# Performance work log

Hardware: AMD Instinct MI355X
Metric: run time of the kernel (lower is better)

## Reference

```python
import jax, jax.numpy as jnp
import numpy as np
from jax import lax

N_NODES = 100000
N_EDGES = 600000  # even: edges stored as consecutive reverse pairs
NODE_F = 64
EDGE_F = 16
EDGE_H = 128
NODE_H = 128
NUM_STEPS = 6


def setup_inputs() -> dict:
    key = jax.random.key(0)
    ks = jax.random.split(key, 16)
    # paired reverse edges: edge 2k is (src,dst), edge 2k+1 is (dst,src)
    src = jax.random.randint(ks[0], (N_EDGES // 2,), 0, N_NODES, dtype=jnp.int32)
    dst = jax.random.randint(ks[1], (N_EDGES // 2,), 0, N_NODES, dtype=jnp.int32)
    from_nodes = jnp.stack([src, dst], axis=1).reshape(-1)
    to_nodes = jnp.stack([dst, src], axis=1).reshape(-1)
    edges = jnp.stack([from_nodes, to_nodes], axis=0)
    return {
        "node_features": jax.random.normal(ks[2], (N_NODES, NODE_F), jnp.float32),
        "edge_features": jax.random.normal(ks[3], (N_EDGES, EDGE_F), jnp.float32),
        "edge_hiddens": jnp.zeros((N_EDGES, EDGE_H), jnp.float32),
        "edges": edges,
        "W1_w": jax.random.normal(ks[4], (NODE_F, EDGE_H), jnp.float32) / np.sqrt(NODE_F),
        "W1_b": jnp.zeros((EDGE_H,), jnp.float32),
        "W2_w": jax.random.normal(ks[5], (EDGE_F, EDGE_H), jnp.float32) / np.sqrt(EDGE_F),
        "W2_b": jnp.zeros((EDGE_H,), jnp.float32),
        "W3_w": jax.random.normal(ks[6], (EDGE_H, EDGE_H), jnp.float32) / np.sqrt(EDGE_H),
        "W3_b": jnp.zeros((EDGE_H,), jnp.float32),
        "U1_w": jax.random.normal(ks[7], (NODE_F, NODE_H), jnp.float32) / np.sqrt(NODE_F),
        "U1_b": jnp.zeros((NODE_H,), jnp.float32),
        "U2_w": jax.random.normal(ks[8], (EDGE_H, NODE_H), jnp.float32) / np.sqrt(EDGE_H),
        "U2_b": jnp.zeros((NODE_H,), jnp.float32),
    }


def reference(node_features, edge_features, edge_hiddens, edges,
              W1_w, W1_b, W2_w, W2_b, W3_w, W3_b, U1_w, U1_b, U2_w, U2_b):
    from_nodes = edges[0]
    to_nodes = edges[1]
    n_edges = edges.shape[1]
    # backlink of edge i is its reverse pair: even i -> i+1, odd i -> i-1
    idx = jnp.arange(n_edges)
    backlink = idx + ((idx + 1) % 2) * 2 - 1

    # loop-invariant terms
    W1_x_u = (node_features @ W1_w + W1_b)[from_nodes]     # [E, EH]
    W2_x_uv = edge_features @ W2_w + W2_b                  # [E, EH]

    def step(h, _):
        # sum edge hiddens by source node, gather back per-edge, drop backlink
        s = jax.ops.segment_sum(h, from_nodes, num_segments=N_NODES)  # [N, EH]
        wu = s[from_nodes] - h[backlink]                               # [E, EH]
        h_new = jax.nn.relu(W1_x_u + W2_x_uv + (wu @ W3_w + W3_b))
        return h_new, None

    edge_h, _ = lax.scan(step, edge_hiddens, None, length=NUM_STEPS)

    U1_x_u = node_features @ U1_w + U1_b                   # [N, NH]
    U2_vu = edge_h @ U2_w + U2_b                           # [E, NH]
    agg = jax.ops.segment_sum(U2_vu, to_nodes, num_segments=N_NODES)
    node_hiddens = jax.nn.relu(U1_x_u + agg)               # [N, NH]
    return node_hiddens
```

## Files before the change

kernel.cpp:

```cpp
#include <hip/hip_runtime.h>
#include <hip/hip_bf16.h>

#define N_NODES 100000
#define N_EDGES 600000
#define SCAN_BLOCKS ((N_NODES + 255) / 256)

typedef __bf16 bf16;
typedef __bf16 bf16x2 __attribute__((ext_vector_type(2)));
typedef __bf16 bf16x4 __attribute__((ext_vector_type(4)));
typedef __bf16 bf16x8 __attribute__((ext_vector_type(8)));
typedef float f32x4 __attribute__((ext_vector_type(4)));

__global__ void deg_hist(const int* __restrict__ from, int* __restrict__ deg, int E) {
    int e = blockIdx.x * blockDim.x + threadIdx.x;
    if (e < E) atomicAdd(&deg[from[e]], 1);
}

__global__ __launch_bounds__(256) void block_sums(
    const int* __restrict__ deg, int* __restrict__ bsum)
{
    __shared__ int s[256];
    int i = blockIdx.x * 256 + threadIdx.x;
    s[threadIdx.x] = (i < N_NODES) ? deg[i] : 0;
    __syncthreads();
    for (int st = 128; st > 0; st >>= 1) {
        if (threadIdx.x < st) s[threadIdx.x] += s[threadIdx.x + st];
        __syncthreads();
    }
    if (threadIdx.x == 0) bsum[blockIdx.x] = s[0];
}

__global__ __launch_bounds__(256) void scan_partials(
    const int* __restrict__ bsum, int* __restrict__ bpref, int* __restrict__ off)
{
    __shared__ int s[SCAN_BLOCKS];
    for (int i = threadIdx.x; i < SCAN_BLOCKS; i += 256) s[i] = bsum[i];
    __syncthreads();
    if (threadIdx.x == 0) {
        int run = 0;
        for (int i = 0; i < SCAN_BLOCKS; i++) { int t = s[i]; s[i] = run; run += t; }
        off[N_NODES] = run;
    }
    __syncthreads();
    for (int i = threadIdx.x; i < SCAN_BLOCKS; i += 256) bpref[i] = s[i];
}

__global__ __launch_bounds__(256) void block_scan(
    const int* __restrict__ deg, const int* __restrict__ bpref,
    int* __restrict__ off, int* __restrict__ cursor)
{
    __shared__ int s[256];
    int i = blockIdx.x * 256 + threadIdx.x;
    int v = (i < N_NODES) ? deg[i] : 0;
    s[threadIdx.x] = v;
    __syncthreads();
    for (int st = 1; st < 256; st <<= 1) {
        int x = (threadIdx.x >= st) ? s[threadIdx.x - st] : 0;
        __syncthreads();
        s[threadIdx.x] += x;
        __syncthreads();
    }
    if (i < N_NODES) {
        int o = bpref[blockIdx.x] + s[threadIdx.x] - v;
        off[i] = o;
        cursor[i] = o;
    }
}

__global__ void scatter_csr(const int* __restrict__ from, int* __restrict__ cursor,
                            int* __restrict__ se, int* __restrict__ rank, int E) {
    int e = blockIdx.x * blockDim.x + threadIdx.x;
    if (e < E) {
        int p = atomicAdd(&cursor[from[e]], 1);
        se[p] = e;
        rank[e] = p;
    }
}

__global__ void make_maps(const int* __restrict__ se, const int* __restrict__ from,
                          const int* __restrict__ rank,
                          int* __restrict__ fromP, int* __restrict__ backP, int E) {
    int i = blockIdx.x * blockDim.x + threadIdx.x;
    if (i < E) {
        int e = se[i];
        fromP[i] = from[e];
        backP[i] = rank[e ^ 1];
    }
}

__global__ __launch_bounds__(256) void node_gemm(
    const float* __restrict__ A, const float* __restrict__ B,
    const float* __restrict__ bias, float* __restrict__ C, int M)
{
    __shared__ float As[16][65];
    __shared__ float Bs[16][128];
    int row0 = blockIdx.x * 64;
    int tid = threadIdx.x;
    int tx = tid & 15, ty = tid >> 4;
    float acc[4][8];
    #pragma unroll
    for (int i = 0; i < 4; i++)
        #pragma unroll
        for (int j = 0; j < 8; j++) acc[i][j] = 0.f;

    for (int kk = 0; kk < 64; kk += 16) {
        int m  = tid >> 2;
        int k4 = (tid & 3) * 4;
        float4 v = make_float4(0.f, 0.f, 0.f, 0.f);
        if (row0 + m < M)
            v = *(const float4*)(A + (size_t)(row0 + m) * 64 + kk + k4);
        As[k4 + 0][m] = v.x; As[k4 + 1][m] = v.y;
        As[k4 + 2][m] = v.z; As[k4 + 3][m] = v.w;
        #pragma unroll
        for (int t = 0; t < 2; t++) {
            int id = tid + t * 256;
            int k = id >> 5, n4 = (id & 31) * 4;
            *(float4*)(&Bs[k][n4]) = *(const float4*)(B + (size_t)(kk + k) * 128 + n4);
        }
        __syncthreads();
        #pragma unroll
        for (int k = 0; k < 16; k++) {
            float a[4], b[8];
            #pragma unroll
            for (int i = 0; i < 4; i++) a[i] = As[k][ty * 4 + i];
            #pragma unroll
            for (int j = 0; j < 8; j++) b[j] = Bs[k][tx + j * 16];
            #pragma unroll
            for (int i = 0; i < 4; i++)
                #pragma unroll
                for (int j = 0; j < 8; j++) acc[i][j] += a[i] * b[j];
        }
        __syncthreads();
    }
    #pragma unroll
    for (int i = 0; i < 4; i++) {
        int r = row0 + ty * 4 + i;
        if (r < M) {
            #pragma unroll
            for (int j = 0; j < 8; j++) {
                int c = tx + j * 16;
                C[(size_t)r * 128 + c] = acc[i][j] + bias[c];
            }
        }
    }
}

__global__ __launch_bounds__(256) void base_sorted(
    const float* __restrict__ nodeW1, const int* __restrict__ fromP,
    const int* __restrict__ se, const float* __restrict__ ef,
    const float* __restrict__ W2, const float* __restrict__ W2b,
    const float* __restrict__ W3b, bf16* __restrict__ baseP)
{
    int tid = threadIdx.x;
    int c0 = (tid & 31) * 4;
    int sub = tid >> 5;
    float4 w[16];
    #pragma unroll
    for (int k = 0; k < 16; k++) w[k] = *(const float4*)(W2 + k * 128 + c0);
    float4 bias;
    {
        float4 a = *(const float4*)(W2b + c0);
        float4 b = *(const float4*)(W3b + c0);
        bias = make_float4(a.x + b.x, a.y + b.y, a.z + b.z, a.w + b.w);
    }
    #pragma unroll 1
    for (int it = 0; it < 64; ++it) {
        int i = blockIdx.x * 512 + it * 8 + sub;
        if (i >= N_EDGES) break;
        const float* efr = ef + (size_t)se[i] * 16;
        float4 nv = *(const float4*)(nodeW1 + (size_t)fromP[i] * 128 + c0);
        float4 acc = make_float4(bias.x + nv.x, bias.y + nv.y,
                                 bias.z + nv.z, bias.w + nv.w);
        #pragma unroll
        for (int k = 0; k < 16; k++) {
            float s = efr[k];
            acc.x += s * w[k].x; acc.y += s * w[k].y;
            acc.z += s * w[k].z; acc.w += s * w[k].w;
        }
        bf16x4 o;
        o[0] = (bf16)acc.x; o[1] = (bf16)acc.y; o[2] = (bf16)acc.z; o[3] = (bf16)acc.w;
        *(bf16x4*)(baseP + (size_t)i * 128 + c0) = o;
    }
}

__global__ __launch_bounds__(256) void prep_weights(
    const float* __restrict__ W3, const float* __restrict__ U2,
    bf16* __restrict__ W3T, bf16* __restrict__ U2T)
{
    int i = blockIdx.x * 256 + threadIdx.x;
    if (i < 128 * 128) {
        int k = i >> 7, n = i & 127;
        W3T[n * 128 + k] = (bf16)W3[k * 128 + n];
        U2T[n * 128 + k] = (bf16)U2[k * 128 + n];
    }
}

__global__ __launch_bounds__(256) void edge_mfma_v3(
    const bf16* __restrict__ baseP, const bf16* __restrict__ gin,
    const float* __restrict__ Sin, const int* __restrict__ fromP,
    const int* __restrict__ backP, const int* __restrict__ off,
    const bf16* __restrict__ BT, bf16* __restrict__ gout,
    float* __restrict__ Sout, int fused, int do_seg, int scatter)
{
    __shared__ bf16 Bsw[128 * 128];
    int tid = threadIdx.x;

    #pragma unroll
    for (int t = 0; t < 8; t++) {
        int c = tid + t * 256;
        int cmr = c & 15;
        int cq  = (c >> 4) & 3;
        int ckt = (c >> 6) & 3;
        int cn  = c >> 8;
        int brow = cn * 16 + cmr;
        int bcol = ckt * 32 + cq * 8;
        *(bf16x8*)&Bsw[(size_t)c * 8] =
            *(const bf16x8*)(BT + (size_t)brow * 128 + bcol);
    }
    __syncthreads();

    int wave = tid >> 6, lane = tid & 63;
    int quad = lane >> 4, mr = lane & 15;

    #pragma unroll 1
    for (int it = 0; it < 4; ++it) {
        int i0 = blockIdx.x * 256 + wave * 64 + it * 16;
        if (i0 >= N_EDGES) break;
        int i = i0 + mr;

        bf16x8 afr[4];
        if (!fused) {
            #pragma unroll
            for (int kt = 0; kt < 4; kt++) {
                bf16x8 bb = *(const bf16x8*)(baseP + (size_t)i * 128 + kt * 32 + quad * 8);
                #pragma unroll
                for (int j = 0; j < 8; j++)
                    afr[kt][j] = (bf16)fmaxf((float)bb[j], 0.f);
            }
        } else {
            const float* sr = Sin + (size_t)fromP[i] * 128;
            const bf16*  gr = gin + (size_t)backP[i] * 128;
            #pragma unroll
            for (int kt = 0; kt < 4; kt++) {
                int c = kt * 32 + quad * 8;
                bf16x8 bb = *(const bf16x8*)(baseP + (size_t)i * 128 + c);
                bf16x8 gg = *(const bf16x8*)(gr + c);
                float4 s0 = *(const float4*)(sr + c);
                float4 s1 = *(const float4*)(sr + c + 4);
                float sv[8] = {s0.x, s0.y, s0.z, s0.w, s1.x, s1.y, s1.z, s1.w};
                #pragma unroll
                for (int j = 0; j < 8; j++) {
                    float v = (float)bb[j] + sv[j] - (float)gg[j];
                    afr[kt][j] = (bf16)fmaxf(v, 0.f);
                }
            }
        }

        f32x4 acc[8];
        #pragma unroll
        for (int n = 0; n < 8; n++) acc[n] = (f32x4){0.f, 0.f, 0.f, 0.f};
        #pragma unroll
        for (int kt = 0; kt < 4; kt++) {
            #pragma unroll
            for (int n = 0; n < 8; n++) {
                bf16x8 b = *(const bf16x8*)&Bsw[(size_t)(((n * 4 + kt) * 64) + lane) * 8];
                acc[n] = __builtin_amdgcn_mfma_f32_16x16x32_bf16(afr[kt], b, acc[n], 0, 0, 0);
            }
        }

        int rbase4 = i0 + quad * 4;
        int orow[4];
        #pragma unroll
        for (int reg = 0; reg < 4; reg++)
            orow[reg] = scatter ? backP[rbase4 + reg] : (rbase4 + reg);

        #pragma unroll
        for (int np = 0; np < 4; np++) {
            int n0 = np * 2;
            #pragma unroll
            for (int reg = 0; reg < 4; reg++) {
                float v0 = acc[n0][reg], v1 = acc[n0 + 1][reg];
                float o0 = __shfl_xor(v0, 1);
                float o1 = __shfl_xor(v1, 1);
                bf16x2 pk;
                int colb;
                if ((mr & 1) == 0) {
                    pk[0] = (bf16)v0; pk[1] = (bf16)o0;
                    colb = n0 * 16 + mr;
                } else {
                    pk[0] = (bf16)o1; pk[1] = (bf16)v1;
                    colb = (n0 + 1) * 16 + (mr ^ 1);
                }
                *(bf16x2*)(gout + (size_t)orow[reg] * 128 + colb) = pk;
            }
        }
    }

    if (do_seg) {
        __syncthreads();
        int rbase = blockIdx.x * 256 + wave * 64;
        int rend  = rbase + 64;
        if (rend > N_EDGES) rend = N_EDGES;
        int r = rbase;
        while (r < rend) {
            int n  = fromP[r];
            int bs = off[n], be = off[n + 1];
            int e  = be < rend ? be : rend;
            float a0 = 0.f, a1 = 0.f;
            for (int j = r; j < e; ++j) {
                bf16x2 v = *(const bf16x2*)(gout + (size_t)j * 128 + lane * 2);
                a0 += (float)v[0];
                a1 += (float)v[1];
            }
            float* sp = Sout + (size_t)n * 128 + lane * 2;
            if (bs >= rbase && be <= rend) {
                *(float2*)sp = make_float2(a0, a1);
            } else {
                atomicAdd(sp, a0);
                atomicAdd(sp + 1, a1);
            }
            r = e;
        }
    }
}

__global__ __launch_bounds__(256) void segsum_final_fused(
    const bf16* __restrict__ gB, const int* __restrict__ off,
    const float* __restrict__ U1x, const float* __restrict__ U2b,
    float* __restrict__ out)
{
    int n = blockIdx.x * 4 + (threadIdx.x >> 6);
    if (n >= N_NODES) return;
    int lane = threadIdx.x & 63;
    int o0 = off[n], o1 = off[n + 1];
    float a0 = 0.f, a1 = 0.f;
    for (int i = o0; i < o1; ++i) {
        bf16x2 v = *(const bf16x2*)(gB + (size_t)i * 128 + lane * 2);
        a0 += (float)v[0];
        a1 += (float)v[1];
    }
    float d = (float)(o1 - o0);
    float2 u = *(const float2*)(U1x + (size_t)n * 128 + lane * 2);
    float2 b = *(const float2*)(U2b + lane * 2);
    float r0 = fmaxf(u.x + a0 + d * b.x, 0.f);
    float r1 = fmaxf(u.y + a1 + d * b.y, 0.f);
    *(float2*)(out + (size_t)n * 128 + lane * 2) = make_float2(r0, r1);
}

extern "C" void kernel_launch(void* const* d_in, const int* in_sizes, int n_in,
                              void* d_out, int out_size, void* d_ws, size_t ws_size,
                              hipStream_t stream) {
    const float* nf  = (const float*)d_in[0];
    const float* ef  = (const float*)d_in[1];
    const int* edges = (const int*)d_in[3];
    const int* from  = edges;
    const float* W1w = (const float*)d_in[4];
    const float* W1b = (const float*)d_in[5];
    const float* W2w = (const float*)d_in[6];
    const float* W2b = (const float*)d_in[7];
    const float* W3w = (const float*)d_in[8];
    const float* W3b = (const float*)d_in[9];
    const float* U1w = (const float*)d_in[10];
    const float* U1b = (const float*)d_in[11];
    const float* U2w = (const float*)d_in[12];
    const float* U2b = (const float*)d_in[13];
    float* out = (float*)d_out;

    const size_t NODE_MAT = (size_t)N_NODES * 128;
    const size_t EDGE_MAT = (size_t)N_EDGES * 128;
    char* w = (char*)d_ws;
    float* nodeW1 = (float*)w; w += NODE_MAT * 4;
    float* SA     = (float*)w; w += NODE_MAT * 4;
    float* SB     = (float*)w; w += NODE_MAT * 4;
    bf16*  baseP  = (bf16*)w;  w += EDGE_MAT * 2;
    bf16*  g0     = (bf16*)w;  w += EDGE_MAT * 2;
    bf16*  g1     = (bf16*)w;  w += EDGE_MAT * 2;
    bf16*  W3T    = (bf16*)w;  w += 128 * 128 * 2;
    bf16*  U2T    = (bf16*)w;  w += 128 * 128 * 2;
    int*   deg    = (int*)w;   w += (size_t)N_NODES * 4;
    int*   off    = (int*)w;   w += (size_t)(N_NODES + 1) * 4;
    int*   cursor = (int*)w;   w += (size_t)N_NODES * 4;
    int*   bsum   = (int*)w;   w += (size_t)SCAN_BLOCKS * 4;
    int*   bpref  = (int*)w;   w += (size_t)SCAN_BLOCKS * 4;
    int*   se     = (int*)w;   w += (size_t)N_EDGES * 4;
    int*   rank   = (int*)w;   w += (size_t)N_EDGES * 4;
    int*   fromP  = (int*)w;   w += (size_t)N_EDGES * 4;
    int*   backP  = (int*)w;   w += (size_t)N_EDGES * 4;

    hipMemsetAsync(deg, 0, (size_t)N_NODES * 4, stream);
    deg_hist<<<(N_EDGES + 255) / 256, 256, 0, stream>>>(from, deg, N_EDGES);
    block_sums<<<SCAN_BLOCKS, 256, 0, stream>>>(deg, bsum);
    scan_partials<<<1, 256, 0, stream>>>(bsum, bpref, off);
    block_scan<<<SCAN_BLOCKS, 256, 0, stream>>>(deg, bpref, off, cursor);
    scatter_csr<<<(N_EDGES + 255) / 256, 256, 0, stream>>>(from, cursor, se, rank, N_EDGES);
    make_maps<<<(N_EDGES + 255) / 256, 256, 0, stream>>>(se, from, rank, fromP, backP, N_EDGES);

    prep_weights<<<(128 * 128 + 255) / 256, 256, 0, stream>>>(W3w, U2w, W3T, U2T);
    node_gemm<<<(N_NODES + 63) / 64, 256, 0, stream>>>(nf, W1w, W1b, nodeW1, N_NODES);
    base_sorted<<<(N_EDGES + 511) / 512, 256, 0, stream>>>(
        nodeW1, fromP, se, ef, W2w, W2b, W3b, baseP);

    const int EGRID = (N_EDGES + 255) / 256;
    const size_t SBYTES = NODE_MAT * 4;

    hipMemsetAsync(SA, 0, SBYTES, stream);
    edge_mfma_v3<<<EGRID, 256, 0, stream>>>(
        baseP, g0, SB, fromP, backP, off, W3T, g0, SA, 0, 1, 0);
    hipMemsetAsync(SB, 0, SBYTES, stream);
    edge_mfma_v3<<<EGRID, 256, 0, stream>>>(
        baseP, g0, SA, fromP, backP, off, W3T, g1, SB, 1, 1, 0);
    hipMemsetAsync(SA, 0, SBYTES, stream);
    edge_mfma_v3<<<EGRID, 256, 0, stream>>>(
        baseP, g1, SB, fromP, backP, off, W3T, g0, SA, 1, 1, 0);
    hipMemsetAsync(SB, 0, SBYTES, stream);
    edge_mfma_v3<<<EGRID, 256, 0, stream>>>(
        baseP, g0, SA, fromP, backP, off, W3T, g1, SB, 1, 1, 0);
    hipMemsetAsync(SA, 0, SBYTES, stream);
    edge_mfma_v3<<<EGRID, 256, 0, stream>>>(
        baseP, g1, SB, fromP, backP, off, W3T, g0, SA, 1, 1, 0);

    edge_mfma_v3<<<EGRID, 256, 0, stream>>>(
        baseP, g0, SA, fromP, backP, off, U2T, g1, SB, 1, 0, 1);

    node_gemm<<<(N_NODES + 63) / 64, 256, 0, stream>>>(nf, U1w, U1b, nodeW1, N_NODES);
    segsum_final_fused<<<(N_NODES + 3) / 4, 256, 0, stream>>>(
        g1, off, nodeW1, U2b, out);
}
```

Baseline: 1.936 ms.

## Fuse segment sum into MFMA epilogue via register-run atomics, gather backlinks in final

Replaces the post-GEMM segment-sum pass, which re-read gout from global memory after a barrier, with a per-thread run-length reduction over the four accumulator rows. Partial sums go straight to the node sums with atomicAdd whenever the source node changes. The final MFMA pass no longer scatters its output through backP. Instead, the final node aggregation kernel gathers rows through backP. This removes one global re-read of the edge hiddens per step and the scattered stores, at the cost of far more float atomics, roughly one per four edges per column instead of only at segment boundaries.

```diff
diff --git a/kernel.cpp b/kernel.cpp
--- a/kernel.cpp
+++ b/kernel.cpp
@@ -195,12 +195,12 @@
     }
 }
 
-__global__ __launch_bounds__(256) void edge_mfma_v3(
+__global__ __launch_bounds__(256) void edge_mfma_v6(
     const bf16* __restrict__ baseP, const bf16* __restrict__ gin,
     const float* __restrict__ Sin, const int* __restrict__ fromP,
-    const int* __restrict__ backP, const int* __restrict__ off,
-    const bf16* __restrict__ BT, bf16* __restrict__ gout,
-    float* __restrict__ Sout, int fused, int do_seg, int scatter)
+    const int* __restrict__ backP, const bf16* __restrict__ BT,
+    bf16* __restrict__ gout, float* __restrict__ Snext,
+    int fused, int do_seg)
 {
     __shared__ bf16 Bsw[128 * 128];
     int tid = threadIdx.x;
@@ -267,12 +267,6 @@
                 acc[n] = __builtin_amdgcn_mfma_f32_16x16x32_bf16(afr[kt], b, acc[n], 0, 0, 0);
             }
         }
-
-        int rbase4 = i0 + quad * 4;
-        int orow[4];
-        #pragma unroll
-        for (int reg = 0; reg < 4; reg++)
-            orow[reg] = scatter ? backP[rbase4 + reg] : (rbase4 + reg);
 
         #pragma unroll
         for (int np = 0; np < 4; np++) {
@@ -291,51 +285,43 @@
                     pk[0] = (bf16)o1; pk[1] = (bf16)v1;
                     colb = (n0 + 1) * 16 + (mr ^ 1);
                 }
-                *(bf16x2*)(gout + (size_t)orow[reg] * 128 + colb) = pk;
-            }
-        }
-    }
-
-    if (do_seg) {
-        __syncthreads();
-        int rbase = blockIdx.x * 256 + wave * 64;
-        int rend  = rbase + 64;
-        if (rend > N_EDGES) rend = N_EDGES;
-        int r = rbase;
-        while (r < rend) {
-            int n  = fromP[r];
-            int bs = off[n], be = off[n + 1];
-            int e  = be < rend ? be : rend;
-            float a0 = 0.f, a1 = 0.f;
-            for (int j = r; j < e; ++j) {
-                bf16x2 v = *(const bf16x2*)(gout + (size_t)j * 128 + lane * 2);
-                a0 += (float)v[0];
-                a1 += (float)v[1];
-            }
-            float* sp = Sout + (size_t)n * 128 + lane * 2;
-            if (bs >= rbase && be <= rend) {
-                *(float2*)sp = make_float2(a0, a1);
-            } else {
-                atomicAdd(sp, a0);
-                atomicAdd(sp + 1, a1);
-            }
-            r = e;
-        }
-    }
-}
-
-__global__ __launch_bounds__(256) void segsum_final_fused(
+                int row = i0 + quad * 4 + reg;
+                *(bf16x2*)(gout + (size_t)row * 128 + colb) = pk;
+            }
+        }
+
+        if (do_seg) {
+            int rbase4 = i0 + quad * 4;
+            int4 nid = *(const int4*)(fromP + rbase4);
+            #pragma unroll
+            for (int n = 0; n < 8; n++) {
+                int col = n * 16 + mr;
+                float run = acc[n][0];
+                if (nid.y == nid.x) run += acc[n][1];
+                else { atomicAdd(Snext + (size_t)nid.x * 128 + col, run); run = acc[n][1]; }
+                if (nid.z == nid.y) run += acc[n][2];
+                else { atomicAdd(Snext + (size_t)nid.y * 128 + col, run); run = acc[n][2]; }
+                if (nid.w == nid.z) run += acc[n][3];
+                else { atomicAdd(Snext + (size_t)nid.z * 128 + col, run); run = acc[n][3]; }
+                atomicAdd(Snext + (size_t)nid.w * 128 + col, run);
+            }
+        }
+    }
+}
+
+__global__ __launch_bounds__(256) void final_gather_out(
     const bf16* __restrict__ gB, const int* __restrict__ off,
-    const float* __restrict__ U1x, const float* __restrict__ U2b,
-    float* __restrict__ out)
+    const int* __restrict__ backP, const float* __restrict__ U1x,
+    const float* __restrict__ U2b, float* __restrict__ out)
 {
     int n = blockIdx.x * 4 + (threadIdx.x >> 6);
     if (n >= N_NODES) return;
     int lane = threadIdx.x & 63;
     int o0 = off[n], o1 = off[n + 1];
     float a0 = 0.f, a1 = 0.f;
-    for (int i = o0; i < o1; ++i) {
-        bf16x2 v = *(const bf16x2*)(gB + (size_t)i * 128 + lane * 2);
+    for (int p = o0; p < o1; ++p) {
+        int e = backP[p];
+        bf16x2 v = *(const bf16x2*)(gB + (size_t)e * 128 + lane * 2);
         a0 += (float)v[0];
         a1 += (float)v[1];
     }
@@ -404,25 +390,24 @@
     const size_t SBYTES = NODE_MAT * 4;
 
     hipMemsetAsync(SA, 0, SBYTES, stream);
-    edge_mfma_v3<<<EGRID, 256, 0, stream>>>(
-        baseP, g0, SB, fromP, backP, off, W3T, g0, SA, 0, 1, 0);
+    edge_mfma_v6<<<EGRID, 256, 0, stream>>>(
+        baseP, g0, SB, fromP, backP, W3T, g0, SA, 0, 1);
     hipMemsetAsync(SB, 0, SBYTES, stream);
-    edge_mfma_v3<<<EGRID, 256, 0, stream>>>(
-        baseP, g0, SA, fromP, backP, off, W3T, g1, SB, 1, 1, 0);
+    edge_mfma_v6<<<EGRID, 256, 0, stream>>>(
+        baseP, g0, SA, fromP, backP, W3T, g1, SB, 1, 1);
     hipMemsetAsync(SA, 0, SBYTES, stream);
-    edge_mfma_v3<<<EGRID, 256, 0, stream>>>(
-        baseP, g1, SB, fromP, backP, off, W3T, g0, SA, 1, 1, 0);
+    edge_mfma_v6<<<EGRID, 256, 0, stream>>>(
+        baseP, g1, SB, fromP, backP, W3T, g0, SA, 1, 1);
     hipMemsetAsync(SB, 0, SBYTES, stream);
-    edge_mfma_v3<<<EGRID, 256, 0, stream>>>(
-        baseP, g0, SA, fromP, backP, off, W3T, g1, SB, 1, 1, 0);
+    edge_mfma_v6<<<EGRID, 256, 0, stream>>>(
+        baseP, g0, SA, fromP, backP, W3T, g1, SB, 1, 1);
     hipMemsetAsync(SA, 0, SBYTES, stream);
-    edge_mfma_v3<<<EGRID, 256, 0, stream>>>(
-        baseP, g1, SB, fromP, backP, off, W3T, g0, SA, 1, 1, 0);
-
-    edge_mfma_v3<<<EGRID, 256, 0, stream>>>(
-        baseP, g0, SA, fromP, backP, off, U2T, g1, SB, 1, 0, 1);
+    edge_mfma_v6<<<EGRID, 256, 0, stream>>>(
+        baseP, g1, SB, fromP, backP, W3T, g0, SA, 1, 1);
+    edge_mfma_v6<<<EGRID, 256, 0, stream>>>(
+        baseP, g0, SA, fromP, backP, U2T, g1, SB, 1, 0);
 
     node_gemm<<<(N_NODES + 63) / 64, 256, 0, stream>>>(nf, U1w, U1b, nodeW1, N_NODES);
-    segsum_final_fused<<<(N_NODES + 3) / 4, 256, 0, stream>>>(
-        g1, off, nodeW1, U2b, out);
-}
+    final_gather_out<<<(N_NODES + 3) / 4, 256, 0, stream>>>(
+        g1, off, backP, nodeW1, U2b, out);
+}
```

Result: faster. 1.846 ms (-4.6%).
